# Optimization experiments

Hardware: AMD Instinct MI355X
Metric: run time of the kernel (lower is better)

## Reference

```python
import jax, jax.numpy as jnp
import numpy as np

B, DE, T = 32, 256, 32
H, W, C = 128, 128, 128  # units == C


def setup_inputs() -> dict:
    key = jax.random.key(0)
    k1, k2, k3 = jax.random.split(key, 3)
    e = jax.random.normal(k1, (B, DE, T), dtype=jnp.float32)
    h = jax.random.normal(k2, (B, H, W, C), dtype=jnp.float32)
    Wd = jax.random.normal(k3, (DE, C), dtype=jnp.float32) * (1.0 / np.sqrt(DE))
    b = jnp.zeros((C,), dtype=jnp.float32)
    return {"e": e, "h": h, "Wd": Wd, "b": b}


def reference(e, h, Wd, b):
    # e: [B, DE, T]  -> dense over DE -> e_: [B, C, T]
    e_ = jnp.einsum('bdt,dc->bct', e, Wd) + b[None, :, None]
    Bh, Hh, Wh, Ch = h.shape
    HW = Hh * Wh
    # h NHWC -> [B, C, HW]
    h1 = h.transpose(0, 3, 1, 2).reshape(Bh, Ch, HW)
    # scores: [B, T, HW], contraction over channels
    s = jnp.einsum('bct,bcn->btn', e_, h1)
    # softmax over T (axis=1)
    beta = jax.nn.softmax(s, axis=1)
    # context: [B, C, HW]
    c = jnp.einsum('bct,btn->bcn', e_, beta)
    # -> [B, HW, C] -> NHWC
    c = c.transpose(0, 2, 1).reshape(Bh, Hh, Wh, Ch)
    return jnp.concatenate([c, h], axis=3)  # [B, H, W, 2C]
```

## Files before the change

kernel.cpp:

```cpp
#include <hip/hip_runtime.h>

typedef float v2f __attribute__((ext_vector_type(2)));

#define B_   32
#define DE_  256
#define T_   32
#define C_   128
#define HW_  16384

#define LSTRIDE 257

__device__ inline v2f vfma2(v2f a, v2f b, v2f c) {
#if __has_builtin(__builtin_elementwise_fma)
    return __builtin_elementwise_fma(a, b, c);
#else
    v2f r; r.x = fmaf(a.x, b.x, c.x); r.y = fmaf(a.y, b.y, c.y); return r;
#endif
}

__global__ __launch_bounds__(256) void dense_e_kernel(
    const float* __restrict__ e, const float* __restrict__ Wd,
    const float* __restrict__ bias, float* __restrict__ ews)
{
    __shared__ float elds[DE_ * T_];
    __shared__ float wlds[DE_ * 16];
    const int b   = blockIdx.y;
    const int cq  = blockIdx.x;
    const int tid = threadIdx.x;

    {
        const float4* erow = (const float4*)(e + ((size_t)b * DE_ + tid) * T_);
        float4* edst = (float4*)(elds + tid * T_);
        #pragma unroll
        for (int i = 0; i < 8; ++i) edst[i] = erow[i];

        const float4* wrow = (const float4*)(Wd + (size_t)tid * C_ + cq * 16);
        float4* wdst = (float4*)(wlds + tid * 16);
        #pragma unroll
        for (int i = 0; i < 4; ++i) wdst[i] = wrow[i];
    }
    __syncthreads();

    const int t  = tid & 31;
    const int c8 = tid >> 5;
    float a0 = 0.f, a1 = 0.f;
    #pragma unroll 8
    for (int d = 0; d < DE_; ++d) {
        float ev = elds[d * T_ + t];
        a0 = fmaf(ev, wlds[d * 16 + c8],     a0);
        a1 = fmaf(ev, wlds[d * 16 + 8 + c8], a1);
    }
    const int c0 = cq * 16 + c8;
    a0 += bias[c0];
    a1 += bias[c0 + 8];
    ews[((size_t)b * C_ + c0)     * T_ + t] = a0;
    ews[((size_t)b * C_ + c0 + 8) * T_ + t] = a1;
}

__global__ __launch_bounds__(256) void attn_fused_kernel(
    const float* __restrict__ h,
    const float* __restrict__ ews,
    float* __restrict__ out)
{
    __shared__ float lds[32 * LSTRIDE];
    const int b   = blockIdx.x >> 6;
    const int n0  = (blockIdx.x & 63) << 8;
    const int tid = threadIdx.x;
    const float* __restrict__ eb = ews + (size_t)b * (C_ * T_);
    const float* __restrict__ hb = h   + ((size_t)b * HW_ + n0) * C_;
    float* __restrict__       ob = out + ((size_t)b * HW_ + n0) * (2 * C_);

    v2f s2[16];
    #pragma unroll
    for (int i = 0; i < 16; ++i) s2[i] = (v2f){0.f, 0.f};

    for (int cb = 0; cb < 4; ++cb) {
        float4 hv[8];
        #pragma unroll
        for (int i = 0; i < 8; ++i) {
            const int idx = i * 256 + tid;
            hv[i] = *(const float4*)(hb + (size_t)(idx >> 3) * C_ + cb * 32 + (idx & 7) * 4);
        }
        #pragma unroll
        for (int i = 0; i < 8; ++i) {
            const int idx = i * 256 + tid;
            const int row = idx >> 3, c4 = idx & 7;
            *(float4*)(ob + (size_t)row * (2 * C_) + C_ + cb * 32 + c4 * 4) = hv[i];
            float* dst = lds + (c4 * 4) * LSTRIDE + row;
            dst[0]           = hv[i].x;
            dst[LSTRIDE]     = hv[i].y;
            dst[2 * LSTRIDE] = hv[i].z;
            dst[3 * LSTRIDE] = hv[i].w;
        }
        __syncthreads();

        const float* ec = eb + (cb * 32) * T_;
        #pragma unroll
        for (int c = 0; c < 32; ++c) {
            const float hc = lds[c * LSTRIDE + tid];
            const v2f* er = (const v2f*)(ec + c * T_);
            const v2f hbv = {hc, hc};
            #pragma unroll
            for (int tp = 0; tp < 16; ++tp) s2[tp] = vfma2(hbv, er[tp], s2[tp]);
        }
        __syncthreads();
    }

    v2f m2 = s2[0];
    #pragma unroll
    for (int i = 1; i < 16; ++i) {
        m2.x = fmaxf(m2.x, s2[i].x);
        m2.y = fmaxf(m2.y, s2[i].y);
    }
    const float m = fmaxf(m2.x, m2.y);
    float l = 0.f;
    #pragma unroll
    for (int i = 0; i < 16; ++i) {
        v2f p;
        p.x = __expf(s2[i].x - m);
        p.y = __expf(s2[i].y - m);
        s2[i] = p;
        l += p.x + p.y;
    }
    const float inv = 1.0f / l;
    #pragma unroll
    for (int i = 0; i < 16; ++i) { s2[i].x *= inv; s2[i].y *= inv; }

    for (int cb = 0; cb < 4; ++cb) {
        #pragma unroll
        for (int c = 0; c < 32; ++c) {
            const v2f* er = (const v2f*)(eb + (size_t)(cb * 32 + c) * T_);
            v2f a = {0.f, 0.f};
            #pragma unroll
            for (int tp = 0; tp < 16; ++tp) a = vfma2(er[tp], s2[tp], a);
            lds[c * LSTRIDE + tid] = a.x + a.y;
        }
        __syncthreads();
        #pragma unroll
        for (int i = 0; i < 8; ++i) {
            const int idx = i * 256 + tid;
            const int row = idx >> 3, c4 = idx & 7;
            const float* src = lds + (c4 * 4) * LSTRIDE + row;
            float4 st = { src[0], src[LSTRIDE], src[2 * LSTRIDE], src[3 * LSTRIDE] };
            *(float4*)(ob + (size_t)row * (2 * C_) + cb * 32 + c4 * 4) = st;
        }
        __syncthreads();
    }
}

extern "C" void kernel_launch(void* const* d_in, const int* in_sizes, int n_in,
                              void* d_out, int out_size, void* d_ws, size_t ws_size,
                              hipStream_t stream) {
    const float* e    = (const float*)d_in[0];
    const float* h    = (const float*)d_in[1];
    const float* Wd   = (const float*)d_in[2];
    const float* bias = (const float*)d_in[3];
    float* ews = (float*)d_ws;
    float* out = (float*)d_out;

    dense_e_kernel<<<dim3(8, 32), 256, 0, stream>>>(e, Wd, bias, ews);
    attn_fused_kernel<<<dim3(32 * (HW_ / 256)), 256, 0, stream>>>(h, ews, out);
}
```

Before: 905.0 us.

## Give each thread two pixels and stage e tiles in LDS for reuse

The attention kernel now runs 128 threads per block, and each thread handles two spatial positions with two score accumulator sets. Each 16-channel slice of e is staged in shared memory with float4 reads, so one e load serves two positions instead of each thread reading e from global memory every time. This raises register pressure and halves threads per block, which may lower occupancy. It also adds more barriers because the channel loop runs in eight smaller chunks.

```diff
diff --git a/kernel.cpp b/kernel.cpp
--- a/kernel.cpp
+++ b/kernel.cpp
@@ -8,7 +8,7 @@
 #define C_   128
 #define HW_  16384
 
-#define LSTRIDE 257
+#define HSTRIDE 257
 
 __device__ inline v2f vfma2(v2f a, v2f b, v2f c) {
 #if __has_builtin(__builtin_elementwise_fma)
@@ -57,12 +57,14 @@
     ews[((size_t)b * C_ + c0 + 8) * T_ + t] = a1;
 }
 
-__global__ __launch_bounds__(256) void attn_fused_kernel(
+__global__ __launch_bounds__(128) void attn_fused_kernel(
     const float* __restrict__ h,
     const float* __restrict__ ews,
     float* __restrict__ out)
 {
-    __shared__ float lds[32 * LSTRIDE];
+    __shared__ float hT[16 * HSTRIDE];
+    __shared__ float es[16 * T_];
+
     const int b   = blockIdx.x >> 6;
     const int n0  = (blockIdx.x & 63) << 8;
     const int tid = threadIdx.x;
@@ -70,79 +72,108 @@
     const float* __restrict__ hb = h   + ((size_t)b * HW_ + n0) * C_;
     float* __restrict__       ob = out + ((size_t)b * HW_ + n0) * (2 * C_);
 
-    v2f s2[16];
+    v2f s0[16], s1[16];
     #pragma unroll
-    for (int i = 0; i < 16; ++i) s2[i] = (v2f){0.f, 0.f};
+    for (int i = 0; i < 16; ++i) { s0[i] = (v2f){0.f, 0.f}; s1[i] = (v2f){0.f, 0.f}; }
 
-    for (int cb = 0; cb < 4; ++cb) {
+    for (int ch = 0; ch < 8; ++ch) {
         float4 hv[8];
         #pragma unroll
         for (int i = 0; i < 8; ++i) {
-            const int idx = i * 256 + tid;
-            hv[i] = *(const float4*)(hb + (size_t)(idx >> 3) * C_ + cb * 32 + (idx & 7) * 4);
+            const int idx = i * 128 + tid;
+            hv[i] = *(const float4*)(hb + (size_t)(idx >> 2) * C_ + ch * 16 + (idx & 3) * 4);
         }
+        ((float4*)es)[tid] = ((const float4*)(eb + ch * 16 * T_))[tid];
         #pragma unroll
         for (int i = 0; i < 8; ++i) {
-            const int idx = i * 256 + tid;
-            const int row = idx >> 3, c4 = idx & 7;
-            *(float4*)(ob + (size_t)row * (2 * C_) + C_ + cb * 32 + c4 * 4) = hv[i];
-            float* dst = lds + (c4 * 4) * LSTRIDE + row;
-            dst[0]           = hv[i].x;
-            dst[LSTRIDE]     = hv[i].y;
-            dst[2 * LSTRIDE] = hv[i].z;
-            dst[3 * LSTRIDE] = hv[i].w;
+            const int idx = i * 128 + tid;
+            const int row = idx >> 2, c4 = idx & 3;
+            *(float4*)(ob + (size_t)row * (2 * C_) + C_ + ch * 16 + c4 * 4) = hv[i];
+            float* d = hT + (c4 * 4) * HSTRIDE + row;
+            d[0]           = hv[i].x;
+            d[HSTRIDE]     = hv[i].y;
+            d[2 * HSTRIDE] = hv[i].z;
+            d[3 * HSTRIDE] = hv[i].w;
         }
         __syncthreads();
 
-        const float* ec = eb + (cb * 32) * T_;
         #pragma unroll
-        for (int c = 0; c < 32; ++c) {
-            const float hc = lds[c * LSTRIDE + tid];
-            const v2f* er = (const v2f*)(ec + c * T_);
-            const v2f hbv = {hc, hc};
+        for (int cl = 0; cl < 16; ++cl) {
+            const float h0 = hT[cl * HSTRIDE + tid];
+            const float h1 = hT[cl * HSTRIDE + 128 + tid];
+            const float4* ec4 = (const float4*)(es + cl * T_);
+            const v2f h0v = {h0, h0}, h1v = {h1, h1};
             #pragma unroll
-            for (int tp = 0; tp < 16; ++tp) s2[tp] = vfma2(hbv, er[tp], s2[tp]);
+            for (int k = 0; k < 8; ++k) {
+                const float4 ef = ec4[k];
+                const v2f eA = {ef.x, ef.y}, eB = {ef.z, ef.w};
+                s0[2 * k]     = vfma2(h0v, eA, s0[2 * k]);
+                s0[2 * k + 1] = vfma2(h0v, eB, s0[2 * k + 1]);
+                s1[2 * k]     = vfma2(h1v, eA, s1[2 * k]);
+                s1[2 * k + 1] = vfma2(h1v, eB, s1[2 * k + 1]);
+            }
         }
         __syncthreads();
     }
 
-    v2f m2 = s2[0];
-    #pragma unroll
-    for (int i = 1; i < 16; ++i) {
-        m2.x = fmaxf(m2.x, s2[i].x);
-        m2.y = fmaxf(m2.y, s2[i].y);
+    {
+        v2f m2 = s0[0];
+        #pragma unroll
+        for (int i = 1; i < 16; ++i) { m2.x = fmaxf(m2.x, s0[i].x); m2.y = fmaxf(m2.y, s0[i].y); }
+        const float m = fmaxf(m2.x, m2.y);
+        float l = 0.f;
+        #pragma unroll
+        for (int i = 0; i < 16; ++i) {
+            v2f p; p.x = __expf(s0[i].x - m); p.y = __expf(s0[i].y - m);
+            s0[i] = p; l += p.x + p.y;
+        }
+        const float inv = 1.0f / l;
+        #pragma unroll
+        for (int i = 0; i < 16; ++i) { s0[i].x *= inv; s0[i].y *= inv; }
     }
-    const float m = fmaxf(m2.x, m2.y);
-    float l = 0.f;
-    #pragma unroll
-    for (int i = 0; i < 16; ++i) {
-        v2f p;
-        p.x = __expf(s2[i].x - m);
-        p.y = __expf(s2[i].y - m);
-        s2[i] = p;
-        l += p.x + p.y;
+    {
+        v2f m2 = s1[0];
+        #pragma unroll
+        for (int i = 1; i < 16; ++i) { m2.x = fmaxf(m2.x, s1[i].x); m2.y = fmaxf(m2.y, s1[i].y); }
+        const float m = fmaxf(m2.x, m2.y);
+        float l = 0.f;
+        #pragma unroll
+        for (int i = 0; i < 16; ++i) {
+            v2f p; p.x = __expf(s1[i].x - m); p.y = __expf(s1[i].y - m);
+            s1[i] = p; l += p.x + p.y;
+        }
+        const float inv = 1.0f / l;
+        #pragma unroll
+        for (int i = 0; i < 16; ++i) { s1[i].x *= inv; s1[i].y *= inv; }
     }
-    const float inv = 1.0f / l;
-    #pragma unroll
-    for (int i = 0; i < 16; ++i) { s2[i].x *= inv; s2[i].y *= inv; }
 
-    for (int cb = 0; cb < 4; ++cb) {
+    for (int ch = 0; ch < 8; ++ch) {
+        ((float4*)es)[tid] = ((const float4*)(eb + ch * 16 * T_))[tid];
+        __syncthreads();
         #pragma unroll
-        for (int c = 0; c < 32; ++c) {
-            const v2f* er = (const v2f*)(eb + (size_t)(cb * 32 + c) * T_);
-            v2f a = {0.f, 0.f};
+        for (int cl = 0; cl < 16; ++cl) {
+            const float4* ec4 = (const float4*)(es + cl * T_);
+            v2f a0 = {0.f, 0.f}, a1 = {0.f, 0.f};
             #pragma unroll
-            for (int tp = 0; tp < 16; ++tp) a = vfma2(er[tp], s2[tp], a);
-            lds[c * LSTRIDE + tid] = a.x + a.y;
+            for (int k = 0; k < 8; ++k) {
+                const float4 ef = ec4[k];
+                const v2f eA = {ef.x, ef.y}, eB = {ef.z, ef.w};
+                a0 = vfma2(eA, s0[2 * k], a0);
+                a0 = vfma2(eB, s0[2 * k + 1], a0);
+                a1 = vfma2(eA, s1[2 * k], a1);
+                a1 = vfma2(eB, s1[2 * k + 1], a1);
+            }
+            hT[cl * HSTRIDE + tid]       = a0.x + a0.y;
+            hT[cl * HSTRIDE + 128 + tid] = a1.x + a1.y;
         }
         __syncthreads();
         #pragma unroll
         for (int i = 0; i < 8; ++i) {
-            const int idx = i * 256 + tid;
-            const int row = idx >> 3, c4 = idx & 7;
-            const float* src = lds + (c4 * 4) * LSTRIDE + row;
-            float4 st = { src[0], src[LSTRIDE], src[2 * LSTRIDE], src[3 * LSTRIDE] };
-            *(float4*)(ob + (size_t)row * (2 * C_) + cb * 32 + c4 * 4) = st;
+            const int idx = i * 128 + tid;
+            const int row = idx >> 2, c4 = idx & 3;
+            const float* src = hT + (c4 * 4) * HSTRIDE + row;
+            float4 st = { src[0], src[HSTRIDE], src[2 * HSTRIDE], src[3 * HSTRIDE] };
+            *(float4*)(ob + (size_t)row * (2 * C_) + ch * 16 + c4 * 4) = st;
         }
         __syncthreads();
     }
@@ -159,5 +190,5 @@
     float* out = (float*)d_out;
 
     dense_e_kernel<<<dim3(8, 32), 256, 0, stream>>>(e, Wd, bias, ews);
-    attn_fused_kernel<<<dim3(32 * (HW_ / 256)), 256, 0, stream>>>(h, ews, out);
+    attn_fused_kernel<<<dim3(32 * (HW_ / 256)), 128, 0, stream>>>(h, ews, out);
 }
```

Result: faster. 866.1 us (-4.3%).
